# Kernel tuning notes

Hardware: AMD Instinct MI355X
Metric: run time of the kernel (lower is better)

## Reference

```python
import jax, jax.numpy as jnp
import numpy as np

DIM = 512
HEADS = 16
WIN = (7, 7)
S = WIN[0] * WIN[1]          # 49 tokens per window
NW = 64                      # windows per image (mask dim)
B_IMG = 32
B = B_IMG * NW               # 2048 total windows
TABLE = (2 * WIN[0] - 1) * (2 * WIN[1] - 1)  # 169


def _relative_position_index():
    ch = np.arange(WIN[0]); cw = np.arange(WIN[1])
    coords = np.stack(np.meshgrid(ch, cw, indexing='ij')).reshape(2, -1)  # [2, S]
    rel = coords[:, :, None] - coords[:, None, :]                          # [2, S, S]
    rel = rel.transpose(1, 2, 0).astype(np.int32)
    rel[:, :, 0] += WIN[0] - 1
    rel[:, :, 1] += WIN[1] - 1
    rel[:, :, 0] *= 2 * WIN[1] - 1
    return rel.sum(-1)  # [S, S], values in [0, TABLE)


def setup_inputs() -> dict:
    key = jax.random.key(0)
    ks = jax.random.split(key, 7)
    return {
        'x': jax.random.normal(ks[0], (B, S, DIM), jnp.float32),
        'mask': jax.random.normal(ks[1], (NW, S, S), jnp.float32),
        'qkv_w': jax.random.normal(ks[2], (DIM, 3 * DIM), jnp.float32) * (DIM ** -0.5),
        'qkv_b': jax.random.normal(ks[3], (3 * DIM,), jnp.float32) * 0.02,
        'proj_w': jax.random.normal(ks[4], (DIM, DIM), jnp.float32) * (DIM ** -0.5),
        'proj_b': jax.random.normal(ks[5], (DIM,), jnp.float32) * 0.02,
        'bias_table': jax.random.normal(ks[6], (TABLE, HEADS), jnp.float32) * 0.02,
        'rel_idx': jnp.asarray(_relative_position_index()),
    }


def reference(x, mask, qkv_w, qkv_b, proj_w, proj_b, bias_table, rel_idx):
    b, s, c = x.shape
    hd = c // HEADS
    scale = hd ** -0.5
    qkv = x @ qkv_w + qkv_b                                   # [B, S, 3C]
    qkv = qkv.reshape(b, s, 3, HEADS, hd).transpose(2, 0, 3, 1, 4)
    q, k, v = qkv[0], qkv[1], qkv[2]                          # [B, H, S, hd]
    attn = jnp.einsum('bhqd,bhkd->bhqk', q * scale, k)        # [B, H, S, S]
    # gathered relative position bias: [S*S, H] -> [H, S, S]
    bias = bias_table[rel_idx.reshape(-1)].reshape(s, s, HEADS).transpose(2, 0, 1)
    attn = attn + bias[None]
    # shifted-window mask add
    nw = mask.shape[0]
    attn = attn.reshape(-1, nw, HEADS, s, s) + mask[None, :, None]
    attn = attn.reshape(-1, HEADS, s, s)
    attn = jax.nn.softmax(attn, axis=-1)
    out = jnp.einsum('bhqk,bhkd->bhqd', attn, v)              # [B, H, S, hd]
    out = out.transpose(0, 2, 1, 3).reshape(b, s, c)
    return out @ proj_w + proj_b
```

## Files before the change

### kernel.cpp

```cpp
#include <hip/hip_runtime.h>


typedef unsigned short u16;
typedef __attribute__((ext_vector_type(8))) short short8;
typedef __attribute__((ext_vector_type(4))) float floatx4;

#define B_WIN 2048
#define SEQ 49
#define DIM 512
#define NHEAD 16
#define HD 32
#define MROWS (B_WIN * SEQ)
#define QTOT 51380224u
#define VOFF 102760448u

__device__ __forceinline__ u16 f2bf(float x) {
    unsigned u = __float_as_uint(x);
    u += 0x7fffu + ((u >> 16) & 1u);
    return (u16)(u >> 16);
}

__device__ __forceinline__ void async_ld16(const void* g, void* l) {
    __builtin_amdgcn_global_load_lds(
        (const __attribute__((address_space(1))) void*)g,
        (__attribute__((address_space(3))) void*)l, 16, 0, 0);
}

__global__ void conv_f32_bf16(const float* __restrict__ in, u16* __restrict__ out, int n4) {
    int id = blockIdx.x * 256 + threadIdx.x;
    if (id >= n4) return;
    float4 v = ((const float4*)in)[id];
    uint2 o;
    o.x = (unsigned)f2bf(v.x) | ((unsigned)f2bf(v.y) << 16);
    o.y = (unsigned)f2bf(v.z) | ((unsigned)f2bf(v.w) << 16);
    *(uint2*)(out + (size_t)id * 4) = o;
}

__global__ void transpose_conv(const float* __restrict__ in, u16* __restrict__ out, int Cn) {
    int id = blockIdx.x * 256 + threadIdx.x;
    if (id >= Cn * 512) return;
    int k = id & 511;
    int n = id >> 9;
    out[id] = f2bf(in[(size_t)k * Cn + n]);
}

__global__ void build_combined(const float* __restrict__ mask, const float* __restrict__ bias_table,
                               const int* __restrict__ rel_idx, float* __restrict__ cmb) {
    int id = blockIdx.x * 256 + threadIdx.x;
    if (id >= 64 * 16 * 2401) return;
    int ij = id % 2401;
    int wh = id / 2401;
    int h = wh & 15, w = wh >> 4;
    cmb[id] = bias_table[rel_idx[ij] * NHEAD + h] + mask[(size_t)w * 2401 + ij];
}

__global__ __launch_bounds__(256, 2)
void gemm_qkv(const u16* __restrict__ A, const u16* __restrict__ Bt,
              const float* __restrict__ bias, u16* __restrict__ qkvp) {
    const int K = 512;
    const int tid  = threadIdx.x;
    const int lane = tid & 63, wave = tid >> 6;
    const int quad = lane >> 4, l16 = lane & 15;
    const int wr = wave >> 1, wc = wave & 1;
    const int m0 = blockIdx.y * 128, n0 = blockIdx.x * 128;

    __shared__ u16 As[128 * 32];
    __shared__ u16 Bs[128 * 32];

    const int f0 = (wave * 2 + 0) * 512 + lane * 8;
    const int f1 = (wave * 2 + 1) * 512 + lane * 8;
    const int r0 = f0 >> 5, c0 = f0 & 31;
    const int r1 = f1 >> 5, c1 = f1 & 31;
    const u16* Ab = A + (size_t)m0 * K;
    const u16* Bb = Bt + (size_t)n0 * K;

    floatx4 acc[4][4] = {};

    for (int kt = 0; kt < K; kt += 32) {
        async_ld16(Ab + (size_t)r0 * K + kt + c0, &As[f0]);
        async_ld16(Ab + (size_t)r1 * K + kt + c1, &As[f1]);
        async_ld16(Bb + (size_t)r0 * K + kt + c0, &Bs[f0]);
        async_ld16(Bb + (size_t)r1 * K + kt + c1, &Bs[f1]);
        __syncthreads();
        short8 af[4], bf[4];
#pragma unroll
        for (int i = 0; i < 4; ++i)
            af[i] = *(const short8*)&As[(wr * 64 + i * 16 + l16) * 32 + quad * 8];
#pragma unroll
        for (int j = 0; j < 4; ++j)
            bf[j] = *(const short8*)&Bs[(wc * 64 + j * 16 + l16) * 32 + quad * 8];
#pragma unroll
        for (int i = 0; i < 4; ++i)
#pragma unroll
            for (int j = 0; j < 4; ++j)
                acc[i][j] = __builtin_amdgcn_mfma_f32_16x16x32_bf16(af[i], bf[j], acc[i][j], 0, 0, 0);
        __syncthreads();
    }

#pragma unroll
    for (int i = 0; i < 4; ++i) {
#pragma unroll
        for (int r = 0; r < 4; ++r) {
            int row = m0 + wr * 64 + i * 16 + quad * 4 + r;
            int b2 = (unsigned)row / 49u;
            int s  = row - b2 * 49;
#pragma unroll
            for (int j = 0; j < 4; ++j) {
                int col = n0 + wc * 64 + j * 16 + l16;
                int c   = col >> 9;
                int rem = col & 511;
                int hh  = rem >> 5, d = rem & 31;
                float val = acc[i][j][r] + bias[col];
                size_t idx;
                if (c < 2) idx = (size_t)c * QTOT + (size_t)(b2 * 16 + hh) * 1568 + s * 32 + d;
                else       idx = VOFF + (size_t)(b2 * 16 + hh) * 2048 + d * 64 + s;
                qkvp[idx] = f2bf(val);
            }
        }
    }
}

__global__ __launch_bounds__(256, 2)
void gemm_bt(const u16* __restrict__ A, const u16* __restrict__ Bt,
             const float* __restrict__ bias, float* __restrict__ Cout,
             int M, int N, int K) {
    const int tid  = threadIdx.x;
    const int lane = tid & 63, wave = tid >> 6;
    const int quad = lane >> 4, l16 = lane & 15;
    const int wr = wave >> 1, wc = wave & 1;
    const int m0 = blockIdx.y * 128, n0 = blockIdx.x * 128;

    __shared__ u16 As[128 * 32];
    __shared__ u16 Bs[128 * 32];

    const int f0 = (wave * 2 + 0) * 512 + lane * 8;
    const int f1 = (wave * 2 + 1) * 512 + lane * 8;
    const int r0 = f0 >> 5, c0 = f0 & 31;
    const int r1 = f1 >> 5, c1 = f1 & 31;
    const u16* Ab = A + (size_t)m0 * K;
    const u16* Bb = Bt + (size_t)n0 * K;

    floatx4 acc[4][4] = {};

    for (int kt = 0; kt < K; kt += 32) {
        async_ld16(Ab + (size_t)r0 * K + kt + c0, &As[f0]);
        async_ld16(Ab + (size_t)r1 * K + kt + c1, &As[f1]);
        async_ld16(Bb + (size_t)r0 * K + kt + c0, &Bs[f0]);
        async_ld16(Bb + (size_t)r1 * K + kt + c1, &Bs[f1]);
        __syncthreads();
        short8 af[4], bf[4];
#pragma unroll
        for (int i = 0; i < 4; ++i)
            af[i] = *(const short8*)&As[(wr * 64 + i * 16 + l16) * 32 + quad * 8];
#pragma unroll
        for (int j = 0; j < 4; ++j)
            bf[j] = *(const short8*)&Bs[(wc * 64 + j * 16 + l16) * 32 + quad * 8];
#pragma unroll
        for (int i = 0; i < 4; ++i)
#pragma unroll
            for (int j = 0; j < 4; ++j)
                acc[i][j] = __builtin_amdgcn_mfma_f32_16x16x32_bf16(af[i], bf[j], acc[i][j], 0, 0, 0);
        __syncthreads();
    }

#pragma unroll
    for (int i = 0; i < 4; ++i) {
#pragma unroll
        for (int j = 0; j < 4; ++j) {
            int col = n0 + wc * 64 + j * 16 + l16;
            float bv = bias[col];
#pragma unroll
            for (int r = 0; r < 4; ++r) {
                int row = m0 + wr * 64 + i * 16 + quad * 4 + r;
                Cout[(size_t)row * N + col] = acc[i][j][r] + bv;
            }
        }
    }
}

__global__ __launch_bounds__(64, 4)
void attn2(const u16* __restrict__ qkvp, const float* __restrict__ cmb,
           u16* __restrict__ out) {
    const int bid = blockIdx.x;
    const int b = bid >> 4, h = bid & 15;
    const int lane = threadIdx.x;
    const int quad = lane >> 4, l16 = lane & 15;

    const u16* qb = qkvp + (size_t)(b * 16 + h) * 1568;
    const u16* kb = qb + QTOT;
    const u16* vb = qkvp + VOFF + (size_t)(b * 16 + h) * 2048;

    __shared__ u16 ps[64 * 72];

    short8 af[4], bfr[4];
#pragma unroll
    for (int i = 0; i < 4; ++i) {
        int r = i * 16 + l16; if (r > 48) r = 48;
        af[i] = *(const short8*)(qb + r * 32 + quad * 8);
    }
#pragma unroll
    for (int j = 0; j < 4; ++j) {
        int n = j * 16 + l16; if (n > 48) n = 48;
        bfr[j] = *(const short8*)(kb + n * 32 + quad * 8);
    }

    const float scale = 0.1767766952966369f;
    const float* cb = cmb + (size_t)((b & 63) * 16 + h) * 2401;

#pragma unroll
    for (int i = 0; i < 4; ++i) {
        floatx4 accS[4] = {};
#pragma unroll
        for (int j = 0; j < 4; ++j)
            accS[j] = __builtin_amdgcn_mfma_f32_16x16x32_bf16(af[i], bfr[j], accS[j], 0, 0, 0);
        const int rbase = i * 16 + quad * 4;
#pragma unroll
        for (int r = 0; r < 4; ++r) {
            int row = rbase + r;
            int rc = row < 48 ? row : 48;
            float x[4];
#pragma unroll
            for (int j = 0; j < 4; ++j) {
                int col = j * 16 + l16;
                x[j] = (col < SEQ) ? accS[j][r] * scale + cb[rc * 49 + col] : -3.0e38f;
            }
            float m = fmaxf(fmaxf(x[0], x[1]), fmaxf(x[2], x[3]));
#pragma unroll
            for (int off = 1; off < 16; off <<= 1) m = fmaxf(m, __shfl_xor(m, off));
            float e[4], s = 0.f;
#pragma unroll
            for (int j = 0; j < 4; ++j) { e[j] = __expf(x[j] - m); s += e[j]; }
#pragma unroll
            for (int off = 1; off < 16; off <<= 1) s += __shfl_xor(s, off);
            float inv = __builtin_amdgcn_rcpf(s);
#pragma unroll
            for (int j = 0; j < 4; ++j)
                ps[row * 72 + j * 16 + l16] = f2bf(e[j] * inv);
        }
    }
    __syncthreads();

    floatx4 accO[4][2] = {};
#pragma unroll
    for (int kt = 0; kt < 2; ++kt) {
        short8 pf[4], vf[2];
#pragma unroll
        for (int i = 0; i < 4; ++i)
            pf[i] = *(const short8*)&ps[(i * 16 + l16) * 72 + kt * 32 + quad * 8];
#pragma unroll
        for (int jn = 0; jn < 2; ++jn)
            vf[jn] = *(const short8*)(vb + (jn * 16 + l16) * 64 + kt * 32 + quad * 8);
#pragma unroll
        for (int i = 0; i < 4; ++i)
#pragma unroll
            for (int jn = 0; jn < 2; ++jn)
                accO[i][jn] = __builtin_amdgcn_mfma_f32_16x16x32_bf16(pf[i], vf[jn], accO[i][jn], 0, 0, 0);
    }

    u16* op = out + (size_t)b * SEQ * DIM + h * HD;
#pragma unroll
    for (int i = 0; i < 4; ++i)
#pragma unroll
        for (int jn = 0; jn < 2; ++jn)
#pragma unroll
            for (int r = 0; r < 4; ++r) {
                int row = i * 16 + quad * 4 + r;
                if (row < SEQ)
                    op[(size_t)row * DIM + jn * 16 + l16] = f2bf(accO[i][jn][r]);
            }
}

extern "C" void kernel_launch(void* const* d_in, const int* in_sizes, int n_in,
                              void* d_out, int out_size, void* d_ws, size_t ws_size,
                              hipStream_t stream) {
    const float* x         = (const float*)d_in[0];
    const float* mask      = (const float*)d_in[1];
    const float* qkv_w     = (const float*)d_in[2];
    const float* qkv_b     = (const float*)d_in[3];
    const float* proj_w    = (const float*)d_in[4];
    const float* proj_b    = (const float*)d_in[5];
    const float* bias_tab  = (const float*)d_in[6];
    const int*   rel_idx   = (const int*)d_in[7];
    float* out = (float*)d_out;

    char* ws = (char*)d_ws;
    u16*   xbf     = (u16*)(ws + 0);
    u16*   qkvp    = (u16*)(ws + 102760448);
    float* cmb     = (float*)(ws + 442499072);
    u16*   wqkv_t  = (u16*)(ws + 452333568);
    u16*   wproj_t = (u16*)(ws + 453906432);

    conv_f32_bf16<<<50176, 256, 0, stream>>>(x, xbf, 12845056);
    transpose_conv<<<3072, 256, 0, stream>>>(qkv_w, wqkv_t, 1536);
    transpose_conv<<<1024, 256, 0, stream>>>(proj_w, wproj_t, 512);
    build_combined<<<9604, 256, 0, stream>>>(mask, bias_tab, rel_idx, cmb);
    gemm_qkv<<<dim3(12, 784), 256, 0, stream>>>(xbf, wqkv_t, qkv_b, qkvp);
    attn2<<<B_WIN * NHEAD, 64, 0, stream>>>(qkvp, cmb, xbf);
    gemm_bt<<<dim3(4, 784), 256, 0, stream>>>(xbf, wproj_t, proj_b, out,
                                              MROWS, 512, 512);
}
```

Measured before the change: 937.4 us.

## Stage QKV epilogue through LDS for coalesced stores and swizzle block order

The QKV GEMM epilogue now writes the bf16 tile into shared memory, then emits 16-byte vectorized stores for Q/K and a column-major pass for the transposed V layout, replacing scattered 2-byte stores. Both GEMMs remap block indices with an XCD-style swizzle (flat&7 stride) so neighbouring tiles land on the same chiplet for L2 reuse. A new kernel zeroes the V padding columns (s=48..63) explicitly. The larger shared buffer (128x136) raises LDS use per block, which may affect occupancy.

Result: faster. 865.9 us (-7.6%).

```diff
diff --git a/kernel.cpp b/kernel.cpp
--- a/kernel.cpp
+++ b/kernel.cpp
@@ -54,6 +54,15 @@
     cmb[id] = bias_table[rel_idx[ij] * NHEAD + h] + mask[(size_t)w * 2401 + ij];
 }
 
+__global__ void zero_vpad(u16* __restrict__ qkvp) {
+    int id = blockIdx.x * 256 + threadIdx.x;
+    if (id >= 2048 * 16 * 32) return;
+    uint4 z = {0u, 0u, 0u, 0u};
+    u16* p = qkvp + VOFF + (size_t)id * 64 + 48;
+    *(uint4*)p = z;
+    *((uint4*)p + 1) = z;
+}
+
 __global__ __launch_bounds__(256, 2)
 void gemm_qkv(const u16* __restrict__ A, const u16* __restrict__ Bt,
               const float* __restrict__ bias, u16* __restrict__ qkvp) {
@@ -62,10 +71,16 @@
     const int lane = tid & 63, wave = tid >> 6;
     const int quad = lane >> 4, l16 = lane & 15;
     const int wr = wave >> 1, wc = wave & 1;
-    const int m0 = blockIdx.y * 128, n0 = blockIdx.x * 128;
-
-    __shared__ u16 As[128 * 32];
-    __shared__ u16 Bs[128 * 32];
+
+    const int flat = blockIdx.y * 12 + blockIdx.x;
+    const int swz  = (flat & 7) * 1176 + (flat >> 3);
+    const int bx = swz % 12;
+    const int by = swz / 12;
+    const int m0 = by * 128, n0 = bx * 128;
+
+    __shared__ u16 smem[128 * 136];
+    u16* As = smem;
+    u16* Bs = smem + 4096;
 
     const int f0 = (wave * 2 + 0) * 512 + lane * 8;
     const int f1 = (wave * 2 + 1) * 512 + lane * 8;
@@ -98,24 +113,50 @@
     }
 
 #pragma unroll
-    for (int i = 0; i < 4; ++i) {
-#pragma unroll
-        for (int r = 0; r < 4; ++r) {
-            int row = m0 + wr * 64 + i * 16 + quad * 4 + r;
-            int b2 = (unsigned)row / 49u;
-            int s  = row - b2 * 49;
-#pragma unroll
-            for (int j = 0; j < 4; ++j) {
-                int col = n0 + wc * 64 + j * 16 + l16;
-                int c   = col >> 9;
-                int rem = col & 511;
-                int hh  = rem >> 5, d = rem & 31;
-                float val = acc[i][j][r] + bias[col];
-                size_t idx;
-                if (c < 2) idx = (size_t)c * QTOT + (size_t)(b2 * 16 + hh) * 1568 + s * 32 + d;
-                else       idx = VOFF + (size_t)(b2 * 16 + hh) * 2048 + d * 64 + s;
-                qkvp[idx] = f2bf(val);
+    for (int j = 0; j < 4; ++j) {
+        const int col = wc * 64 + j * 16 + l16;
+        const float bv = bias[n0 + col];
+#pragma unroll
+        for (int i = 0; i < 4; ++i)
+#pragma unroll
+            for (int r = 0; r < 4; ++r) {
+                const int row = wr * 64 + i * 16 + quad * 4 + r;
+                smem[row * 136 + col] = f2bf(acc[i][j][r] + bv);
             }
+    }
+    __syncthreads();
+
+    if (n0 < 1024) {
+        const int c   = n0 >> 9;
+        const int hh0 = (n0 & 511) >> 5;
+        u16* base = qkvp + (size_t)c * QTOT;
+#pragma unroll
+        for (int it = 0; it < 8; ++it) {
+            const int idx  = it * 256 + tid;
+            const int row  = idx >> 4;
+            const int hb   = (idx >> 2) & 3;
+            const int part = idx & 3;
+            short8 v = *(const short8*)&smem[row * 136 + hb * 32 + part * 8];
+            const int rg = m0 + row;
+            const int b2 = (int)((unsigned)rg / 49u);
+            const int s  = rg - b2 * 49;
+            *(short8*)(base + (size_t)(b2 * 16 + hh0 + hb) * 1568 + s * 32 + part * 8) = v;
+        }
+    } else {
+        const int hh0 = (n0 - 1024) >> 5;
+        u16* base = qkvp + VOFF;
+#pragma unroll 16
+        for (int it = 0; it < 64; ++it) {
+            const int idx = it * 256 + tid;
+            const int col = idx >> 7;
+            const int row = idx & 127;
+            const u16 v = smem[row * 136 + col];
+            const int rg = m0 + row;
+            const int b2 = (int)((unsigned)rg / 49u);
+            const int s  = rg - b2 * 49;
+            const int hh = hh0 + (col >> 5);
+            const int d  = col & 31;
+            base[(size_t)(b2 * 16 + hh) * 2048 + d * 64 + s] = v;
         }
     }
 }
@@ -128,7 +169,14 @@
     const int lane = tid & 63, wave = tid >> 6;
     const int quad = lane >> 4, l16 = lane & 15;
     const int wr = wave >> 1, wc = wave & 1;
-    const int m0 = blockIdx.y * 128, n0 = blockIdx.x * 128;
+
+    const int nbx = gridDim.x, nby = gridDim.y;
+    const int total = nbx * nby;
+    const int flat = blockIdx.y * nbx + blockIdx.x;
+    const int swz = ((total & 7) == 0) ? ((flat & 7) * (total >> 3) + (flat >> 3)) : flat;
+    const int bx = swz % nbx;
+    const int by = swz / nbx;
+    const int m0 = by * 128, n0 = bx * 128;
 
     __shared__ u16 As[128 * 32];
     __shared__ u16 Bs[128 * 32];
@@ -294,6 +342,7 @@
     transpose_conv<<<3072, 256, 0, stream>>>(qkv_w, wqkv_t, 1536);
     transpose_conv<<<1024, 256, 0, stream>>>(proj_w, wproj_t, 512);
     build_combined<<<9604, 256, 0, stream>>>(mask, bias_tab, rel_idx, cmb);
+    zero_vpad<<<4096, 256, 0, stream>>>(qkvp);
     gemm_qkv<<<dim3(12, 784), 256, 0, stream>>>(xbf, wqkv_t, qkv_b, qkvp);
     attn2<<<B_WIN * NHEAD, 64, 0, stream>>>(qkvp, cmb, xbf);
     gemm_bt<<<dim3(4, 784), 256, 0, stream>>>(xbf, wproj_t, proj_b, out,
```
